# Performance work log

Measured on AMD Instinct MI355X. Metric: run time of the kernel, lower is better.

The kernel has to match this reference:

```python
import jax, jax.numpy as jnp
import numpy as np

COMPRESSION = 2

def setup_inputs() -> dict:
    key = jax.random.key(0)
    k = jax.random.split(key, 5)
    B, H, W, C, Ci = 8, 56, 56, 256, 128
    return {
        "x": jax.random.normal(k[0], (B, H, W, C), dtype=jnp.float32),
        "w_theta": jax.random.normal(k[1], (C, Ci), dtype=jnp.float32) * (2.0 / C) ** 0.5,
        "w_phi": jax.random.normal(k[2], (C, Ci), dtype=jnp.float32) * (2.0 / C) ** 0.5,
        "w_g": jax.random.normal(k[3], (C, Ci), dtype=jnp.float32) * (2.0 / C) ** 0.5,
        "w_final": jax.random.normal(k[4], (Ci, C), dtype=jnp.float32) * (2.0 / Ci) ** 0.5,
    }

def _maxpool1d(z, pool):
    # z: [B, N, Ci]; non-overlapping max pool along N (Keras MaxPool1D default stride=pool)
    B, N, Ci = z.shape
    return z[:, : (N // pool) * pool].reshape(B, N // pool, pool, Ci).max(axis=2)

def reference(x, w_theta, w_phi, w_g, w_final):
    B, H, W, C = x.shape
    Ci = w_theta.shape[1]
    N = H * W
    xf = x.reshape(B, N, C)
    # 1x1 convs == per-position matmuls
    theta = xf @ w_theta                      # [B, N, Ci]
    phi = _maxpool1d(xf @ w_phi, COMPRESSION)  # [B, N/2, Ci]
    g = _maxpool1d(xf @ w_g, COMPRESSION)      # [B, N/2, Ci]
    f = jnp.einsum('bnc,bmc->bnm', theta, phi)  # [B, N, N/2]
    f = jax.nn.softmax(f, axis=-1)
    y = jnp.einsum('bnm,bmc->bnc', f, g)        # [B, N, Ci]
    z = y @ w_final                              # [B, N, C]
    return x + z.reshape(B, H, W, C)
```

## Files before the change

### kernel.cpp

```cpp
#include <hip/hip_runtime.h>

typedef _Float16 f16x8 __attribute__((ext_vector_type(8)));
typedef _Float16 f16x4 __attribute__((ext_vector_type(4)));
typedef short s16x4 __attribute__((ext_vector_type(4)));
typedef float f32x4 __attribute__((ext_vector_type(4)));

#define MFMA_K32(a, b, c) __builtin_amdgcn_mfma_f32_16x16x32_f16(a, b, c, 0, 0, 0)
#define MFMA_BF(a, b, c)  __builtin_amdgcn_mfma_f32_16x16x16bf16_1k(a, b, c, 0, 0, 0)
#define MFMA_F16(a, b, c) __builtin_amdgcn_mfma_f32_16x16x16f16(a, b, c, 0, 0, 0)


__device__ __forceinline__ f16x8 ld8f(const float* __restrict__ p) {
    f32x4 a = *(const f32x4*)p;
    f32x4 b = *(const f32x4*)(p + 4);
    f16x8 r;
    r[0] = (_Float16)a[0]; r[1] = (_Float16)a[1];
    r[2] = (_Float16)a[2]; r[3] = (_Float16)a[3];
    r[4] = (_Float16)b[0]; r[5] = (_Float16)b[1];
    r[6] = (_Float16)b[2]; r[7] = (_Float16)b[3];
    return r;
}
__device__ __forceinline__ unsigned f2bf_rne(float f) {
    unsigned u = __float_as_uint(f);
    return (u + 0x7FFFu + ((u >> 16) & 1u)) >> 16;
}
__device__ __forceinline__ int bfpack_rtz(float lo, float hi) {
    return (int)((__float_as_uint(hi) & 0xFFFF0000u) | (__float_as_uint(lo) >> 16));
}

__global__ __launch_bounds__(256) void k_prep(
    const float* __restrict__ wt, const float* __restrict__ wp,
    const float* __restrict__ wg, const float* __restrict__ wf,
    _Float16* __restrict__ wt_f, _Float16* __restrict__ wfT_f) {
    int i = blockIdx.x * 256 + threadIdx.x;
    if (i < 12288) {
        int w    = i >> 12;
        int rem  = i & 4095;
        int ctkc = rem >> 6;
        int l    = rem & 63;
        const float* src = (w == 0) ? wt : (w == 1) ? wp : wg;
        const float* s = src + ((ctkc & 7) * 32 + (l >> 4) * 8) * 128
                             + (ctkc >> 3) * 16 + (l & 15);
        f16x8 v;
#pragma unroll
        for (int jj = 0; jj < 8; ++jj) v[jj] = (_Float16)s[jj * 128];
        *(f16x8*)(wt_f + i * 8) = v;
    } else {
        int j    = i - 12288;
        int ct   = j >> 8;
        int rem  = j & 255;
        int qt   = rem >> 2;
        int kc2e = rem & 3;
        int col  = ct * 16 + (qt & 15);
        int qq   = qt >> 4;
        f16x8 v;
#pragma unroll
        for (int jp = 0; jp < 8; ++jp) {
            int Ci = (kc2e * 2 + (jp >> 2)) * 16 + qq * 4 + (jp & 3);
            v[jp] = (_Float16)wf[Ci * 256 + col];
        }
        *(f16x8*)(wfT_f + j * 8) = v;
    }
}

__global__ __launch_bounds__(256) void k_proj(
    const float* __restrict__ x,
    const _Float16* __restrict__ wt_f,
    _Float16* __restrict__ theta_f,
    _Float16* __restrict__ phi_f,
    short* __restrict__ g_f)
{
    const int w    = blockIdx.y;
    const int wave = threadIdx.x >> 6;
    const int lane = threadIdx.x & 63;
    const int q = lane >> 4, t = lane & 15;
    const int tt = blockIdx.x * 4 + wave;

    __shared__ __align__(16) _Float16 Wl[32768];
    {
        const _Float16* src = wt_f + w * 32768;
#pragma unroll
        for (int j = 0; j < 16; ++j) {
            const int o8 = (j * 256 + threadIdx.x) * 8;
            *(f16x8*)(Wl + o8) = *(const f16x8*)(src + o8);
        }
    }
    __syncthreads();

    const int mrow = tt * 16 + t;
    f16x8 af[8];
#pragma unroll
    for (int kc = 0; kc < 8; ++kc)
        af[kc] = ld8f(x + mrow * 256 + kc * 32 + q * 8);

    const f32x4 zero = {0.f, 0.f, 0.f, 0.f};
    f32x4 acc[8];
#pragma unroll
    for (int ct = 0; ct < 8; ++ct) acc[ct] = zero;

    if (w == 2) {
#pragma unroll
        for (int ct = 0; ct < 8; ++ct) {
            const _Float16* Wc = Wl + (ct * 8) * 512 + lane * 8;
#pragma unroll
            for (int kc = 0; kc < 8; ++kc)
                acc[ct] = MFMA_K32(af[kc], *(const f16x8*)(Wc + kc * 512), acc[ct]);
        }
    } else {
#pragma unroll
        for (int ct = 0; ct < 8; ++ct) {
            const _Float16* Wc = Wl + (ct * 8) * 512 + lane * 8;
#pragma unroll
            for (int kc = 0; kc < 8; ++kc)
                acc[ct] = MFMA_K32(*(const f16x8*)(Wc + kc * 512), af[kc], acc[ct]);
        }
    }

    if (w == 0) {
        _Float16* tb = theta_f + tt * 2048;
#pragma unroll
        for (int ct = 0; ct < 8; ++ct) {
            f16x4 v;
#pragma unroll
            for (int r = 0; r < 4; ++r) v[r] = (_Float16)acc[ct][r];
            const int off = (ct >> 1) * 512
                          + (((ct & 1) * 2 + (q >> 1)) * 16 + t) * 8 + 4 * (q & 1);
            *(f16x4*)(tb + off) = v;
        }
        return;
    }

    const int b     = tt / 196;
    const int tl    = tt - b * 196;
    const int chunk = tl >> 2;
    const int sub   = tl & 3;

    if (w == 1) {
        _Float16* pcb = phi_f + (b * 49 + chunk) * 4096;
#pragma unroll
        for (int ct = 0; ct < 8; ++ct) {
            f32x4 pm;
#pragma unroll
            for (int r = 0; r < 4; ++r)
                pm[r] = fmaxf(acc[ct][r], __shfl_xor(acc[ct][r], 1));
            if (!(t & 1)) {
                f16x4 v;
#pragma unroll
                for (int r = 0; r < 4; ++r) v[r] = (_Float16)pm[r];
                const int off = ((sub >> 1) * 4 + (ct >> 1)) * 512
                              + ((((ct & 1) * 2 + (q >> 1)) * 16)
                                 + (sub & 1) * 8 + (t >> 1)) * 8 + 4 * (q & 1);
                *(f16x4*)(pcb + off) = v;
            }
        }
    } else {
        const int h   = sub >> 1;
        short* gcb = g_f + (b * 49 + chunk) * 4096;
        const int qv  = (sub & 1) * 2 + (q >> 1);
        const int jj0 = (q & 1) * 2;
#pragma unroll
        for (int ct = 0; ct < 8; ++ct) {
            unsigned lo = f2bf_rne(fmaxf(acc[ct][0], acc[ct][1]));
            unsigned hi = f2bf_rne(fmaxf(acc[ct][2], acc[ct][3]));
            *(unsigned*)(gcb + (ct * 2 + h) * 256 + (qv * 16 + t) * 4 + jj0) = lo | (hi << 16);
        }
    }
}

__global__ __launch_bounds__(256) void k_attn(
    const _Float16* __restrict__ theta_f,
    const _Float16* __restrict__ phi_f,
    const short* __restrict__ g_f,
    const _Float16* __restrict__ wfT_f,
    const float* __restrict__ x,
    float* __restrict__ out)
{
    const int blk  = blockIdx.x;
    const int b    = blk & 7;
    const int blkm = blk >> 3;
    const int wave = threadIdx.x >> 6;
    const int lane = threadIdx.x & 63;
    const int q = lane >> 4, t = lane & 15;
    const int m = wave >> 1;
    const int h = wave & 1;

    __shared__ __align__(16) _Float16 kv[2][8192];
    __shared__ float lred[2][64];

    const int tIdx0 = b * 196 + blkm * 2;
    const _Float16* ph = phi_f + b * 200704;
    const _Float16* gt = (const _Float16*)(g_f + b * 200704);

    f16x8 qf[4];
#pragma unroll
    for (int kc = 0; kc < 4; ++kc)
        qf[kc] = *(const f16x8*)(theta_f + (tIdx0 + m) * 2048 + kc * 512 + lane * 8);

    const f32x4 zero = {0.f, 0.f, 0.f, 0.f};
    f32x4 o[8];
#pragma unroll
    for (int ct = 0; ct < 8; ++ct) o[ct] = zero;
    float lsum = 0.f;
    const float L2E = 1.44269504f, SHIFT = 104.0f;

    const _Float16* src0 = (wave < 2) ? (ph + wave * 2048) : (gt + (wave - 2) * 2048);
    const int doff = wave * 2048;

    f16x8 sr[4];
#pragma unroll
    for (int j = 0; j < 4; ++j)
        sr[j] = *(const f16x8*)(src0 + j * 512 + lane * 8);
#pragma unroll
    for (int j = 0; j < 4; ++j)
        *(f16x8*)(&kv[0][doff + j * 512 + lane * 8]) = sr[j];
    __syncthreads();

#pragma unroll 1
    for (int i = 0; i < 49; ++i) {
        if (i + 1 < 49) {
            const _Float16* s = src0 + (i + 1) * 4096;
#pragma unroll
            for (int j = 0; j < 4; ++j)
                sr[j] = *(const f16x8*)(s + j * 512 + lane * 8);
        }

        const _Float16* buf = &kv[i & 1][0];
        f32x4 st = zero;
#pragma unroll
        for (int kc = 0; kc < 4; ++kc) {
            f16x8 a = *(const f16x8*)(buf + (h * 4 + kc) * 512 + lane * 8);
            st = MFMA_K32(a, qf[kc], st);
        }

        f32x4 pv;
#pragma unroll
        for (int r = 0; r < 4; ++r)
            pv[r] = exp2f(st[r] * L2E - SHIFT);
        lsum += (pv[0] + pv[1]) + (pv[2] + pv[3]);
        union { int i2[2]; s16x4 v; } u;
        u.i2[0] = bfpack_rtz(pv[0], pv[1]);
        u.i2[1] = bfpack_rtz(pv[2], pv[3]);

#pragma unroll
        for (int ct = 0; ct < 8; ++ct) {
            s16x4 vf = *(const s16x4*)(buf + 4096 + (ct * 2 + h) * 256 + lane * 4);
            o[ct] = MFMA_BF(vf, u.v, o[ct]);
        }

        if (i + 1 < 49) {
            _Float16* d = &kv[(i + 1) & 1][doff];
#pragma unroll
            for (int j = 0; j < 4; ++j)
                *(f16x8*)(d + j * 512 + lane * 8) = sr[j];
        }
        __syncthreads();
    }

    float* cb = (float*)&kv[0][0];
    if (h == 1) {
#pragma unroll
        for (int ct = 0; ct < 8; ++ct)
            *(f32x4*)&cb[m * 2048 + ct * 256 + lane * 4] = o[ct];
        lred[m][lane] = lsum;
    }
    __syncthreads();
    if (h == 0) {
#pragma unroll
        for (int ct = 0; ct < 8; ++ct)
            o[ct] += *(const f32x4*)&cb[m * 2048 + ct * 256 + lane * 4];
        lsum += lred[m][lane];
#pragma unroll
        for (int ct = 0; ct < 8; ++ct)
            *(f32x4*)&cb[m * 2048 + ct * 256 + lane * 4] = o[ct];
        lred[m][lane] = lsum;
    }
    __syncthreads();
    if (h == 1) {
#pragma unroll
        for (int ct = 0; ct < 8; ++ct)
            o[ct] = *(const f32x4*)&cb[m * 2048 + ct * 256 + lane * 4];
        lsum = lred[m][lane];
    }

    float lf = lsum;
    lf += __shfl_xor(lf, 16);
    lf += __shfl_xor(lf, 32);
    const float inv = 1.0f / lf;

    f16x4 yf[8];
#pragma unroll
    for (int ct = 0; ct < 8; ++ct)
#pragma unroll
        for (int r = 0; r < 4; ++r)
            yf[ct][r] = (_Float16)(o[ct][r] * inv);

    const int row = (tIdx0 + m) * 16 + t;
#pragma unroll 2
    for (int ci = 0; ci < 8; ++ci) {
        const int ctile = h * 8 + ci;
        union { f16x8 v8; f16x4 v4[2]; } w[4];
#pragma unroll
        for (int pp = 0; pp < 4; ++pp)
            w[pp].v8 = *(const f16x8*)(wfT_f + ctile * 2048 + lane * 32 + pp * 8);
        f32x4 acc = zero;
#pragma unroll
        for (int kc2 = 0; kc2 < 8; ++kc2)
            acc = MFMA_F16(w[kc2 >> 1].v4[kc2 & 1], yf[kc2], acc);
        const int col = ctile * 16 + q * 4;
        f32x4 xv = *(const f32x4*)(x + row * 256 + col);
        *(f32x4*)(out + row * 256 + col) = acc + xv;
    }
}

extern "C" void kernel_launch(void* const* d_in, const int* in_sizes, int n_in,
                              void* d_out, int out_size, void* d_ws, size_t ws_size,
                              hipStream_t stream) {
    const float* x  = (const float*)d_in[0];
    const float* wt = (const float*)d_in[1];
    const float* wp = (const float*)d_in[2];
    const float* wg = (const float*)d_in[3];
    const float* wf = (const float*)d_in[4];
    float* out = (float*)d_out;

    _Float16* ws      = (_Float16*)d_ws;
    _Float16* wt_f    = ws;
    _Float16* wfT_f   = ws + 98304;
    _Float16* theta_f = ws + 131072;
    _Float16* phi_f   = ws + 3342336;
    short*    g_f     = (short*)(ws + 4947968);

    k_prep<<<dim3(64),      256, 0, stream>>>(wt, wp, wg, wf, wt_f, wfT_f);
    k_proj<<<dim3(392, 3),  256, 0, stream>>>(x, wt_f, theta_f, phi_f, g_f);
    k_attn<<<dim3(784),     256, 0, stream>>>(theta_f, phi_f, g_f, wfT_f, x, out);
}
```

Baseline: 150.8 us.

## Restructure projection kernel to stage x in LDS and share across three weights

The projection kernel previously launched one block per (row-tile group, weight) pair, with each block copying a 64KB weight slice into LDS and reading x straight from global memory, so x was read three times. Now each block stages a 32-row x tile into padded LDS once, and its waves cover the six (tile, weight) combinations, reading weight fragments directly from global/L2. This cuts redundant x reads and the per-block weight staging. In exchange the work is uneven (six units over four waves, so two waves do double work) and weight loads now come through the cache rather than LDS.

```diff
diff --git a/kernel.cpp b/kernel.cpp
--- a/kernel.cpp
+++ b/kernel.cpp
@@ -10,16 +10,6 @@
 #define MFMA_F16(a, b, c) __builtin_amdgcn_mfma_f32_16x16x16f16(a, b, c, 0, 0, 0)
 
 
-__device__ __forceinline__ f16x8 ld8f(const float* __restrict__ p) {
-    f32x4 a = *(const f32x4*)p;
-    f32x4 b = *(const f32x4*)(p + 4);
-    f16x8 r;
-    r[0] = (_Float16)a[0]; r[1] = (_Float16)a[1];
-    r[2] = (_Float16)a[2]; r[3] = (_Float16)a[3];
-    r[4] = (_Float16)b[0]; r[5] = (_Float16)b[1];
-    r[6] = (_Float16)b[2]; r[7] = (_Float16)b[3];
-    return r;
-}
 __device__ __forceinline__ unsigned f2bf_rne(float f) {
     unsigned u = __float_as_uint(f);
     return (u + 0x7FFFu + ((u >> 16) & 1u)) >> 16;
@@ -70,99 +60,115 @@
     _Float16* __restrict__ phi_f,
     short* __restrict__ g_f)
 {
-    const int w    = blockIdx.y;
-    const int wave = threadIdx.x >> 6;
-    const int lane = threadIdx.x & 63;
+    const int blk  = blockIdx.x;
+    const int tid  = threadIdx.x;
+    const int wave = tid >> 6;
+    const int lane = tid & 63;
     const int q = lane >> 4, t = lane & 15;
-    const int tt = blockIdx.x * 4 + wave;
-
-    __shared__ __align__(16) _Float16 Wl[32768];
-    {
-        const _Float16* src = wt_f + w * 32768;
-#pragma unroll
-        for (int j = 0; j < 16; ++j) {
-            const int o8 = (j * 256 + threadIdx.x) * 8;
-            *(f16x8*)(Wl + o8) = *(const f16x8*)(src + o8);
-        }
+
+    __shared__ __align__(16) float xs[32 * 260];
+
+    const float* xsrc = x + blk * 32 * 256;
+#pragma unroll
+    for (int r = 0; r < 8; ++r) {
+        const int c   = r * 256 + tid;
+        const int row = c >> 6, col4 = c & 63;
+        *(f32x4*)(xs + row * 260 + col4 * 4) = *(const f32x4*)(xsrc + c * 4);
     }
     __syncthreads();
 
-    const int mrow = tt * 16 + t;
-    f16x8 af[8];
-#pragma unroll
-    for (int kc = 0; kc < 8; ++kc)
-        af[kc] = ld8f(x + mrow * 256 + kc * 32 + q * 8);
-
     const f32x4 zero = {0.f, 0.f, 0.f, 0.f};
-    f32x4 acc[8];
-#pragma unroll
-    for (int ct = 0; ct < 8; ++ct) acc[ct] = zero;
-
-    if (w == 2) {
-#pragma unroll
-        for (int ct = 0; ct < 8; ++ct) {
-            const _Float16* Wc = Wl + (ct * 8) * 512 + lane * 8;
-#pragma unroll
-            for (int kc = 0; kc < 8; ++kc)
-                acc[ct] = MFMA_K32(af[kc], *(const f16x8*)(Wc + kc * 512), acc[ct]);
-        }
-    } else {
-#pragma unroll
-        for (int ct = 0; ct < 8; ++ct) {
-            const _Float16* Wc = Wl + (ct * 8) * 512 + lane * 8;
-#pragma unroll
-            for (int kc = 0; kc < 8; ++kc)
-                acc[ct] = MFMA_K32(*(const f16x8*)(Wc + kc * 512), af[kc], acc[ct]);
-        }
-    }
-
-    if (w == 0) {
-        _Float16* tb = theta_f + tt * 2048;
-#pragma unroll
-        for (int ct = 0; ct < 8; ++ct) {
-            f16x4 v;
-#pragma unroll
-            for (int r = 0; r < 4; ++r) v[r] = (_Float16)acc[ct][r];
-            const int off = (ct >> 1) * 512
-                          + (((ct & 1) * 2 + (q >> 1)) * 16 + t) * 8 + 4 * (q & 1);
-            *(f16x4*)(tb + off) = v;
-        }
-        return;
-    }
-
-    const int b     = tt / 196;
-    const int tl    = tt - b * 196;
-    const int chunk = tl >> 2;
-    const int sub   = tl & 3;
-
-    if (w == 1) {
-        _Float16* pcb = phi_f + (b * 49 + chunk) * 4096;
-#pragma unroll
-        for (int ct = 0; ct < 8; ++ct) {
-            f32x4 pm;
-#pragma unroll
-            for (int r = 0; r < 4; ++r)
-                pm[r] = fmaxf(acc[ct][r], __shfl_xor(acc[ct][r], 1));
-            if (!(t & 1)) {
+
+#pragma unroll 1
+    for (int u = wave; u < 6; u += 4) {
+        const int tloc = (u >= 3) ? 1 : 0;
+        const int w    = u - tloc * 3;
+        const int tt   = blk * 2 + tloc;
+
+        f16x8 af[8];
+#pragma unroll
+        for (int kc = 0; kc < 8; ++kc) {
+            const float* p = xs + (tloc * 16 + t) * 260 + kc * 32 + q * 8;
+            f32x4 a = *(const f32x4*)p;
+            f32x4 b = *(const f32x4*)(p + 4);
+            f16x8 v;
+            v[0] = (_Float16)a[0]; v[1] = (_Float16)a[1];
+            v[2] = (_Float16)a[2]; v[3] = (_Float16)a[3];
+            v[4] = (_Float16)b[0]; v[5] = (_Float16)b[1];
+            v[6] = (_Float16)b[2]; v[7] = (_Float16)b[3];
+            af[kc] = v;
+        }
+
+        f32x4 acc[8];
+#pragma unroll
+        for (int ct = 0; ct < 8; ++ct) acc[ct] = zero;
+
+        if (w == 2) {
+#pragma unroll
+            for (int ct = 0; ct < 8; ++ct) {
+                const _Float16* Wc = wt_f + ((2 * 8 + ct) * 8) * 512 + lane * 8;
+#pragma unroll
+                for (int kc = 0; kc < 8; ++kc)
+                    acc[ct] = MFMA_K32(af[kc], *(const f16x8*)(Wc + kc * 512), acc[ct]);
+            }
+        } else {
+#pragma unroll
+            for (int ct = 0; ct < 8; ++ct) {
+                const _Float16* Wc = wt_f + ((w * 8 + ct) * 8) * 512 + lane * 8;
+#pragma unroll
+                for (int kc = 0; kc < 8; ++kc)
+                    acc[ct] = MFMA_K32(*(const f16x8*)(Wc + kc * 512), af[kc], acc[ct]);
+            }
+        }
+
+        if (w == 0) {
+            _Float16* tb = theta_f + tt * 2048;
+#pragma unroll
+            for (int ct = 0; ct < 8; ++ct) {
                 f16x4 v;
 #pragma unroll
-                for (int r = 0; r < 4; ++r) v[r] = (_Float16)pm[r];
-                const int off = ((sub >> 1) * 4 + (ct >> 1)) * 512
-                              + ((((ct & 1) * 2 + (q >> 1)) * 16)
-                                 + (sub & 1) * 8 + (t >> 1)) * 8 + 4 * (q & 1);
-                *(f16x4*)(pcb + off) = v;
-            }
-        }
-    } else {
-        const int h   = sub >> 1;
-        short* gcb = g_f + (b * 49 + chunk) * 4096;
-        const int qv  = (sub & 1) * 2 + (q >> 1);
-        const int jj0 = (q & 1) * 2;
-#pragma unroll
-        for (int ct = 0; ct < 8; ++ct) {
-            unsigned lo = f2bf_rne(fmaxf(acc[ct][0], acc[ct][1]));
-            unsigned hi = f2bf_rne(fmaxf(acc[ct][2], acc[ct][3]));
-            *(unsigned*)(gcb + (ct * 2 + h) * 256 + (qv * 16 + t) * 4 + jj0) = lo | (hi << 16);
+                for (int r = 0; r < 4; ++r) v[r] = (_Float16)acc[ct][r];
+                const int off = (ct >> 1) * 512
+                              + (((ct & 1) * 2 + (q >> 1)) * 16 + t) * 8 + 4 * (q & 1);
+                *(f16x4*)(tb + off) = v;
+            }
+            continue;
+        }
+
+        const int b     = tt / 196;
+        const int tl    = tt - b * 196;
+        const int chunk = tl >> 2;
+        const int sub   = tl & 3;
+
+        if (w == 1) {
+            _Float16* pcb = phi_f + (b * 49 + chunk) * 4096;
+#pragma unroll
+            for (int ct = 0; ct < 8; ++ct) {
+                f32x4 pm;
+#pragma unroll
+                for (int r = 0; r < 4; ++r)
+                    pm[r] = fmaxf(acc[ct][r], __shfl_xor(acc[ct][r], 1));
+                if (!(t & 1)) {
+                    f16x4 v;
+#pragma unroll
+                    for (int r = 0; r < 4; ++r) v[r] = (_Float16)pm[r];
+                    const int off = ((sub >> 1) * 4 + (ct >> 1)) * 512
+                                  + ((((ct & 1) * 2 + (q >> 1)) * 16)
+                                     + (sub & 1) * 8 + (t >> 1)) * 8 + 4 * (q & 1);
+                    *(f16x4*)(pcb + off) = v;
+                }
+            }
+        } else {
+            const int h   = sub >> 1;
+            short* gcb = g_f + (b * 49 + chunk) * 4096;
+            const int qv  = (sub & 1) * 2 + (q >> 1);
+            const int jj0 = (q & 1) * 2;
+#pragma unroll
+            for (int ct = 0; ct < 8; ++ct) {
+                unsigned lo = f2bf_rne(fmaxf(acc[ct][0], acc[ct][1]));
+                unsigned hi = f2bf_rne(fmaxf(acc[ct][2], acc[ct][3]));
+                *(unsigned*)(gcb + (ct * 2 + h) * 256 + (qv * 16 + t) * 4 + jj0) = lo | (hi << 16);
+            }
         }
     }
 }
@@ -329,7 +335,7 @@
     _Float16* phi_f   = ws + 3342336;
     short*    g_f     = (short*)(ws + 4947968);
 
-    k_prep<<<dim3(64),      256, 0, stream>>>(wt, wp, wg, wf, wt_f, wfT_f);
-    k_proj<<<dim3(392, 3),  256, 0, stream>>>(x, wt_f, theta_f, phi_f, g_f);
-    k_attn<<<dim3(784),     256, 0, stream>>>(theta_f, phi_f, g_f, wfT_f, x, out);
-}
+    k_prep<<<dim3(64),  256, 0, stream>>>(wt, wp, wg, wf, wt_f, wfT_f);
+    k_proj<<<dim3(784), 256, 0, stream>>>(x, wt_f, theta_f, phi_f, g_f);
+    k_attn<<<dim3(784), 256, 0, stream>>>(theta_f, phi_f, g_f, wfT_f, x, out);
+}
```

New measurement: 157.9 us. +4.7%, slower.
